# Performance work log

Hardware: AMD Instinct MI355X
Metric: run time of the kernel (lower is better)

The kernel has to match this reference:

```python
import jax, jax.numpy as jnp
import numpy as np

D = 512
H = 8
DH = D // H
DFF = 2048
SLOTS = 1024
TOPK = 5
LN_EPS = 1e-5
NORM_EPS = 1e-12


def setup_inputs() -> dict:
    key = jax.random.key(0)
    ks = jax.random.split(key, 12)
    B, S = 8, 1024
    inp = {
        "src": jax.random.normal(ks[0], (B, S, D), dtype=jnp.float32),
        # MultiheadAttention params (torch layout: in_proj [3D, D], out_proj [D, D])
        "in_proj_w": jax.random.normal(ks[1], (3 * D, D), dtype=jnp.float32) * 0.02,
        "in_proj_b": jnp.zeros((3 * D,), dtype=jnp.float32),
        "out_proj_w": jax.random.normal(ks[2], (D, D), dtype=jnp.float32) * 0.02,
        "out_proj_b": jnp.zeros((D,), dtype=jnp.float32),
        # BPBookMemory params
        "memory": jax.random.normal(ks[3], (SLOTS, D), dtype=jnp.float32),
        "retrieval_scale": jnp.asarray(0.1, dtype=jnp.float32),
        # LayerNorms
        "ln1_g": jnp.ones((D,), dtype=jnp.float32),
        "ln1_b": jnp.zeros((D,), dtype=jnp.float32),
        "ln2_g": jnp.ones((D,), dtype=jnp.float32),
        "ln2_b": jnp.zeros((D,), dtype=jnp.float32),
        # FFN (torch Linear layout: [out, in])
        "w1": jax.random.normal(ks[4], (DFF, D), dtype=jnp.float32) * 0.02,
        "b1": jnp.zeros((DFF,), dtype=jnp.float32),
        "w2": jax.random.normal(ks[5], (D, DFF), dtype=jnp.float32) * 0.02,
        "b2": jnp.zeros((D,), dtype=jnp.float32),
    }
    return inp


def _layer_norm(x, g, b):
    mu = jnp.mean(x, axis=-1, keepdims=True)
    var = jnp.var(x, axis=-1, keepdims=True)
    return (x - mu) * jax.lax.rsqrt(var + LN_EPS) * g + b


def _l2_normalize(x):
    n = jnp.linalg.norm(x, axis=-1, keepdims=True)
    return x / jnp.maximum(n, NORM_EPS)


def _forward(src, in_proj_w, in_proj_b, out_proj_w, out_proj_b,
             memory, retrieval_scale, ln1_g, ln1_b, ln2_g, ln2_b,
             w1, b1, w2, b2):
    B, S, _ = src.shape
    # ---- pre-norm self-attention ----
    h = _layer_norm(src, ln1_g, ln1_b)
    qkv = h @ in_proj_w.T + in_proj_b            # [B,S,3D]
    q, k, v = jnp.split(qkv, 3, axis=-1)
    q = q.reshape(B, S, H, DH)
    k = k.reshape(B, S, H, DH)
    v = v.reshape(B, S, H, DH)
    scores = jnp.einsum("bqhd,bkhd->bhqk", q, k) / jnp.sqrt(jnp.float32(DH))
    attn = jax.nn.softmax(scores, axis=-1)
    ctx = jnp.einsum("bhqk,bkhd->bqhd", attn, v).reshape(B, S, D)
    attn_out = ctx @ out_proj_w.T + out_proj_b
    src = src + attn_out
    # ---- BP-Book memory: cosine sim -> topk -> softmax -> gather -> weighted sum ----
    xn = _l2_normalize(src)                      # [B,S,D]
    mn = _l2_normalize(memory)                   # [SLOTS,D]
    sim = xn @ mn.T                              # [B,S,SLOTS]
    topk_scores, topk_idx = jax.lax.top_k(sim, TOPK)
    w = jax.nn.softmax(topk_scores, axis=-1)     # [B,S,TOPK]
    retrieved = memory[topk_idx]                 # [B,S,TOPK,D]
    weighted = jnp.einsum("bskd,bsk->bsd", retrieved, w)
    src = src + retrieval_scale * weighted
    # ---- FFN ----
    h = _layer_norm(src, ln2_g, ln2_b)
    ffn = jax.nn.gelu(h @ w1.T + b1, approximate=False) @ w2.T + b2
    return src + ffn


def reference(src, in_proj_w, in_proj_b, out_proj_w, out_proj_b,
              memory, retrieval_scale, ln1_g, ln1_b, ln2_g, ln2_b,
              w1, b1, w2, b2):
    return _forward(src, in_proj_w, in_proj_b, out_proj_w, out_proj_b,
                    memory, retrieval_scale, ln1_g, ln1_b, ln2_g, ln2_b,
                    w1, b1, w2, b2)
```

## Files before the change

kernel.cpp:

```cpp
#include <hip/hip_runtime.h>
#include <math.h>

#define D_ 512
#define H_ 8
#define DFF_ 2048
#define SLOTS_ 1024
#define TOPK_ 5
#define NCAND_ 8
#define NTOK_ 8192
#define SEQ_ 1024
#define LN_EPS_ 1e-5f

typedef __attribute__((ext_vector_type(8))) short bf16x8;
typedef __attribute__((ext_vector_type(4))) float f32x4;
typedef __attribute__((ext_vector_type(4))) unsigned u32x4;

__device__ inline void split2(float x, unsigned short& hi, unsigned short& lo) {
    unsigned u = __builtin_bit_cast(unsigned, x);
    hi = (unsigned short)(u >> 16);
    float h = __builtin_bit_cast(float, u & 0xFFFF0000u);
    float rem = x - h;
    lo = (unsigned short)(__builtin_bit_cast(unsigned, rem) >> 16);
}

__device__ __forceinline__ void gld16(const void* g, void* l) {
    __builtin_amdgcn_global_load_lds(
        (const __attribute__((address_space(1))) void*)g,
        (__attribute__((address_space(3))) void*)l, 16, 0, 0);
}

__device__ __forceinline__ int SW7(int r) { return (r ^ (r >> 3)) & 7; }
__device__ __forceinline__ const bf16x8* frag(const unsigned short* p, int r, int c) {
    return (const bf16x8*)(p + r * 64 + ((c ^ SW7(r)) << 3));
}

__global__ __launch_bounds__(256) void split_kernel(
    const float* __restrict__ x, unsigned short* __restrict__ hi,
    unsigned short* __restrict__ lo, int n)
{
    const int i = (blockIdx.x * 256 + threadIdx.x) * 4;
    if (i >= n) return;
    const float4 v = *(const float4*)(x + i);
    const float vv[4] = {v.x, v.y, v.z, v.w};
    unsigned short h[4], l[4];
#pragma unroll
    for (int e = 0; e < 4; ++e) split2(vv[e], h[e], l[e]);
    hi[i + 0] = h[0]; hi[i + 1] = h[1]; hi[i + 2] = h[2]; hi[i + 3] = h[3];
    if (lo) { lo[i + 0] = l[0]; lo[i + 1] = l[1]; lo[i + 2] = l[2]; lo[i + 3] = l[3]; }
}

template <int WLO>
__global__ __launch_bounds__(256) void ln_kernel(
    const float* __restrict__ x, const float* __restrict__ g,
    const float* __restrict__ be, unsigned short* __restrict__ yh,
    unsigned short* __restrict__ yl)
{
    const int row = blockIdx.x;
    const int t = threadIdx.x;
    const float a = x[(size_t)row * D_ + t];
    const float b = x[(size_t)row * D_ + t + 256];
    float s = a + b;
    float ss = a * a + b * b;
#pragma unroll
    for (int off = 32; off; off >>= 1) {
        s += __shfl_xor(s, off);
        ss += __shfl_xor(ss, off);
    }
    __shared__ float rs[4], rss[4];
    if ((t & 63) == 0) { rs[t >> 6] = s; rss[t >> 6] = ss; }
    __syncthreads();
    s = rs[0] + rs[1] + rs[2] + rs[3];
    ss = rss[0] + rss[1] + rss[2] + rss[3];
    const float mu = s * (1.0f / D_);
    const float var = ss * (1.0f / D_) - mu * mu;
    const float r = rsqrtf(var + LN_EPS_);
    const float y0 = (a - mu) * r * g[t] + be[t];
    const float y1 = (b - mu) * r * g[t + 256] + be[t + 256];
    unsigned short h0, l0, h1, l1;
    split2(y0, h0, l0);
    split2(y1, h1, l1);
    yh[(size_t)row * D_ + t] = h0;
    yh[(size_t)row * D_ + t + 256] = h1;
    if (WLO) {
        yl[(size_t)row * D_ + t] = l0;
        yl[(size_t)row * D_ + t + 256] = l1;
    }
}

__global__ __launch_bounds__(64) void mn_kernel(
    const float* __restrict__ mem, float* __restrict__ mn,
    unsigned short* __restrict__ mnh, unsigned short* __restrict__ mnl)
{
    const int row = blockIdx.x;
    const int lane = threadIdx.x;
    float v[8];
    float ss = 0.0f;
#pragma unroll
    for (int j = 0; j < 8; ++j) {
        v[j] = mem[(size_t)row * D_ + j * 64 + lane];
        ss += v[j] * v[j];
    }
#pragma unroll
    for (int off = 32; off; off >>= 1) ss += __shfl_xor(ss, off);
    const float inv = 1.0f / fmaxf(sqrtf(ss), 1e-12f);
#pragma unroll
    for (int j = 0; j < 8; ++j) {
        const float y = v[j] * inv;
        mn[(size_t)row * D_ + j * 64 + lane] = y;
        unsigned short h, l;
        split2(y, h, l);
        mnh[(size_t)row * D_ + j * 64 + lane] = h;
        mnl[(size_t)row * D_ + j * 64 + lane] = l;
    }
}

__global__ __launch_bounds__(64) void rownorm_kernel(
    const float* __restrict__ x, float* __restrict__ invn)
{
    const int row = blockIdx.x;
    const int lane = threadIdx.x;
    float ss = 0.0f;
#pragma unroll
    for (int j = 0; j < 8; ++j) {
        const float v = x[(size_t)row * D_ + j * 64 + lane];
        ss += v * v;
    }
#pragma unroll
    for (int off = 32; off; off >>= 1) ss += __shfl_xor(ss, off);
    if (lane == 0) invn[row] = 1.0f / fmaxf(sqrtf(ss), 1e-12f);
}

enum { EP_QKV = 0, EP_OUTPROJ = 1, EP_SIM = 2, EP_FFN1 = 3, EP_FFN2 = 4 };

template <int SPLIT, int MODE>
__global__ __launch_bounds__(256) void gemm_mf(
    const unsigned short* __restrict__ Ahg, const unsigned short* __restrict__ Alg,
    const unsigned short* __restrict__ Bhg, const unsigned short* __restrict__ Blg,
    const float* __restrict__ bias, const float* __restrict__ res,
    const float* __restrict__ rowscale, float* __restrict__ C,
    unsigned short* __restrict__ Ch, unsigned short* __restrict__ Cl,
    int M, int N, int K)
{
    __shared__ __align__(16) unsigned short sm[(SPLIT == 3 ? 4 : 2) * 8192];
    unsigned short* Ah = sm;
    unsigned short* Al = sm + 8192;
    unsigned short* Bh = sm + (SPLIT == 3 ? 16384 : 8192);
    unsigned short* Bl = sm + 24576;

    const int tid = threadIdx.x;
    const int lane = tid & 63;
    const int w = tid >> 6;
    const int wr = w >> 1, wc = w & 1;
    const int g = lane >> 4, ln = lane & 15;
    const int m0 = blockIdx.x * 128, n0 = blockIdx.y * 128;
    const int lrow8 = lane >> 3, lchunk = lane & 7;

    const unsigned short* gsrc;
    unsigned short* lds;
    int rbase, rofs, nblk;
    if (SPLIT == 3) {
        nblk = 16; rofs = 0;
        if (w == 0)      { gsrc = Ahg; lds = Ah; rbase = m0; }
        else if (w == 1) { gsrc = Alg; lds = Al; rbase = m0; }
        else if (w == 2) { gsrc = Bhg; lds = Bh; rbase = n0; }
        else             { gsrc = Blg; lds = Bl; rbase = n0; }
    } else {
        nblk = 8; rofs = (w & 1) * 64;
        if (w < 2) { gsrc = Ahg; lds = Ah; rbase = m0; }
        else       { gsrc = Bhg; lds = Bh; rbase = n0; }
    }

    f32x4 acc[4][4];
#pragma unroll
    for (int i = 0; i < 4; ++i)
#pragma unroll
        for (int j = 0; j < 4; ++j) acc[i][j] = (f32x4){0.f, 0.f, 0.f, 0.f};

    for (int k0 = 0; k0 < K; k0 += 64) {
#pragma unroll
        for (int blk = 0; blk < nblk; ++blk) {
            const int row = rofs + blk * 8 + lrow8;
            const int sc = lchunk ^ SW7(row);
            gld16(gsrc + (size_t)(rbase + row) * K + k0 + sc * 8,
                  lds + (rofs + blk * 8) * 64);
        }
        __syncthreads();

#pragma unroll
        for (int ks = 0; ks < 2; ++ks) {
            bf16x8 a_h[4], a_l[4], b_h[4], b_l[4];
#pragma unroll
            for (int mi = 0; mi < 4; ++mi) {
                a_h[mi] = *frag(Ah, wr * 64 + mi * 16 + ln, ks * 4 + g);
                if (SPLIT == 3) a_l[mi] = *frag(Al, wr * 64 + mi * 16 + ln, ks * 4 + g);
            }
#pragma unroll
            for (int ni = 0; ni < 4; ++ni) {
                b_h[ni] = *frag(Bh, wc * 64 + ni * 16 + ln, ks * 4 + g);
                if (SPLIT == 3) b_l[ni] = *frag(Bl, wc * 64 + ni * 16 + ln, ks * 4 + g);
            }
#pragma unroll
            for (int mi = 0; mi < 4; ++mi)
#pragma unroll
                for (int ni = 0; ni < 4; ++ni) {
                    acc[mi][ni] = __builtin_amdgcn_mfma_f32_16x16x32_bf16(
                        a_h[mi], b_h[ni], acc[mi][ni], 0, 0, 0);
                    if (SPLIT == 3) {
                        acc[mi][ni] = __builtin_amdgcn_mfma_f32_16x16x32_bf16(
                            a_h[mi], b_l[ni], acc[mi][ni], 0, 0, 0);
                        acc[mi][ni] = __builtin_amdgcn_mfma_f32_16x16x32_bf16(
                            a_l[mi], b_h[ni], acc[mi][ni], 0, 0, 0);
                    }
                }
        }
        __syncthreads();
    }

#pragma unroll
    for (int mi = 0; mi < 4; ++mi) {
#pragma unroll
        for (int ni = 0; ni < 4; ++ni) {
            const int gn = n0 + wc * 64 + ni * 16 + ln;
            const float bz = (MODE == EP_SIM) ? 0.0f : bias[gn];
#pragma unroll
            for (int r2 = 0; r2 < 4; ++r2) {
                const int gm = m0 + wr * 64 + mi * 16 + g * 4 + r2;
                float v = acc[mi][ni][r2];
                if (MODE == EP_SIM) {
                    v *= rowscale[gm];
                    C[(size_t)gm * N + gn] = v;
                } else if (MODE == EP_QKV) {
                    v += bz;
                    if (gn < D_) v *= 0.125f;
                    unsigned short h16, l16;
                    split2(v, h16, l16);
                    Ch[(size_t)gm * N + gn] = h16;
                    Cl[(size_t)gm * N + gn] = l16;
                } else if (MODE == EP_OUTPROJ) {
                    v += bz + res[(size_t)gm * N + gn];
                    C[(size_t)gm * N + gn] = v;
                    unsigned short h16, l16;
                    split2(v, h16, l16);
                    Ch[(size_t)gm * N + gn] = h16;
                    Cl[(size_t)gm * N + gn] = l16;
                } else if (MODE == EP_FFN1) {
                    v += bz;
                    v = 0.5f * v * (1.0f + erff(v * 0.70710678118654752f));
                    unsigned short h16, l16;
                    split2(v, h16, l16);
                    Ch[(size_t)gm * N + gn] = h16;
                } else {
                    v += bz + res[(size_t)gm * N + gn];
                    C[(size_t)gm * N + gn] = v;
                }
            }
        }
    }
}

__global__ __launch_bounds__(256, 2) void attn_kernel(
    const unsigned short* __restrict__ qkvh, const unsigned short* __restrict__ qkvl,
    unsigned short* __restrict__ ctxh, unsigned short* __restrict__ ctxl)
{
    const int id = blockIdx.x;
    const int bh = id & 63;
    const int qt = id >> 6;
    const int b = bh >> 3, h = bh & 7;
    const int tok0 = b * SEQ_ + qt * 128;
    const int kbase0 = b * SEQ_;
    const int tid = threadIdx.x;
    const int lane = tid & 63;
    const int w = tid >> 6;
    const int ln = lane & 15, g = lane >> 4;
    const int lrow8 = lane >> 3, lchunk = lane & 7;

    __shared__ __align__(16) unsigned char smb[65536];
    unsigned*       PP  = (unsigned*)smb;
    unsigned short* Qh  = (unsigned short*)smb;
    unsigned short* Ql  = (unsigned short*)(smb + 16384);
    unsigned short* Kh  = (unsigned short*)(smb + 32768);
    unsigned short* Kl  = (unsigned short*)(smb + 40960);
    unsigned short* Vth = (unsigned short*)(smb + 49152);
    unsigned short* Vtl = (unsigned short*)(smb + 57344);

    const int qoff = h * 64, koff = 512 + h * 64, voff = 1024 + h * 64;

#pragma unroll
    for (int blk = 0; blk < 4; ++blk) {
        const int row = w * 32 + blk * 8 + lrow8;
        const int sc = lchunk ^ SW7(row);
        gld16(qkvh + (size_t)(tok0 + row) * 1536 + qoff + sc * 8,
              Qh + (w * 32 + blk * 8) * 64);
        gld16(qkvl + (size_t)(tok0 + row) * 1536 + qoff + sc * 8,
              Ql + (w * 32 + blk * 8) * 64);
    }
    __syncthreads();
    bf16x8 qfh[2][2], qfl[2][2];
#pragma unroll
    for (int mi = 0; mi < 2; ++mi)
#pragma unroll
        for (int ks = 0; ks < 2; ++ks) {
            qfh[mi][ks] = *frag(Qh, w * 32 + mi * 16 + ln, ks * 4 + g);
            qfl[mi][ks] = *frag(Ql, w * 32 + mi * 16 + ln, ks * 4 + g);
        }

    f32x4 o[2][4];
#pragma unroll
    for (int mi = 0; mi < 2; ++mi)
#pragma unroll
        for (int ni = 0; ni < 4; ++ni) o[mi][ni] = (f32x4){0.f, 0.f, 0.f, 0.f};
    float mrow[2][4], lrow[2][4];
#pragma unroll
    for (int mi = 0; mi < 2; ++mi)
#pragma unroll
        for (int r2 = 0; r2 < 4; ++r2) { mrow[mi][r2] = -INFINITY; lrow[mi][r2] = 0.f; }

    const int p2 = tid & 31, dc = tid >> 5;

    for (int kt = 0; kt < 16; ++kt) {
        const int kb2 = kbase0 + kt * 64;
#pragma unroll
        for (int blk = 0; blk < 2; ++blk) {
            const int row = w * 16 + blk * 8 + lrow8;
            const int sc = lchunk ^ SW7(row);
            gld16(qkvh + (size_t)(kb2 + row) * 1536 + koff + sc * 8,
                  Kh + (w * 16 + blk * 8) * 64);
            gld16(qkvl + (size_t)(kb2 + row) * 1536 + koff + sc * 8,
                  Kl + (w * 16 + blk * 8) * 64);
        }
        {
            const size_t b0 = (size_t)(kb2 + 2 * p2) * 1536 + voff + dc * 8;
            const bf16x8 h0 = *(const bf16x8*)(qkvh + b0);
            const bf16x8 h1 = *(const bf16x8*)(qkvh + b0 + 1536);
            const bf16x8 l0 = *(const bf16x8*)(qkvl + b0);
            const bf16x8 l1 = *(const bf16x8*)(qkvl + b0 + 1536);
#pragma unroll
            for (int j = 0; j < 8; ++j) {
                const int d = dc * 8 + j;
                const int idx = d * 64 + (((p2 >> 2) ^ SW7(d)) << 3) + ((p2 & 3) << 1);
                *(unsigned*)&Vth[idx] = (unsigned)(unsigned short)h0[j]
                                      | ((unsigned)(unsigned short)h1[j] << 16);
                *(unsigned*)&Vtl[idx] = (unsigned)(unsigned short)l0[j]
                                      | ((unsigned)(unsigned short)l1[j] << 16);
            }
        }
        __syncthreads();

        f32x4 s[2][4];
#pragma unroll
        for (int mi = 0; mi < 2; ++mi)
#pragma unroll
            for (int ni = 0; ni < 4; ++ni) s[mi][ni] = (f32x4){0.f, 0.f, 0.f, 0.f};
#pragma unroll
        for (int ks = 0; ks < 2; ++ks) {
            bf16x8 kbh[4], kbl[4];
#pragma unroll
            for (int ni = 0; ni < 4; ++ni) {
                kbh[ni] = *frag(Kh, ni * 16 + ln, ks * 4 + g);
                kbl[ni] = *frag(Kl, ni * 16 + ln, ks * 4 + g);
            }
#pragma unroll
            for (int mi = 0; mi < 2; ++mi)
#pragma unroll
                for (int ni = 0; ni < 4; ++ni) {
                    s[mi][ni] = __builtin_amdgcn_mfma_f32_16x16x32_bf16(qfh[mi][ks], kbh[ni], s[mi][ni], 0, 0, 0);
                    s[mi][ni] = __builtin_amdgcn_mfma_f32_16x16x32_bf16(qfh[mi][ks], kbl[ni], s[mi][ni], 0, 0, 0);
                    s[mi][ni] = __builtin_amdgcn_mfma_f32_16x16x32_bf16(qfl[mi][ks], kbh[ni], s[mi][ni], 0, 0, 0);
                }
        }

        float tm[2][4];
#pragma unroll
        for (int mi = 0; mi < 2; ++mi)
#pragma unroll
            for (int r2 = 0; r2 < 4; ++r2)
                tm[mi][r2] = fmaxf(fmaxf(s[mi][0][r2], s[mi][1][r2]),
                                   fmaxf(s[mi][2][r2], s[mi][3][r2]));
#pragma unroll
        for (int off = 1; off < 16; off <<= 1)
#pragma unroll
            for (int mi = 0; mi < 2; ++mi)
#pragma unroll
                for (int r2 = 0; r2 < 4; ++r2)
                    tm[mi][r2] = fmaxf(tm[mi][r2], __shfl_xor(tm[mi][r2], off));

        float alpha[2][4], psum[2][4];
#pragma unroll
        for (int mi = 0; mi < 2; ++mi)
#pragma unroll
            for (int r2 = 0; r2 < 4; ++r2) {
                const float mnew = fmaxf(mrow[mi][r2], tm[mi][r2]);
                alpha[mi][r2] = __expf(mrow[mi][r2] - mnew);
                mrow[mi][r2] = mnew;
                psum[mi][r2] = 0.f;
            }
#pragma unroll
        for (int mi = 0; mi < 2; ++mi)
#pragma unroll
            for (int ni = 0; ni < 4; ++ni)
#pragma unroll
                for (int r2 = 0; r2 < 4; ++r2) {
                    const float p = __expf(s[mi][ni][r2] - mrow[mi][r2]);
                    psum[mi][r2] += p;
                    unsigned short h16, l16;
                    split2(p, h16, l16);
                    const int prow = w * 32 + mi * 16 + g * 4 + r2;
                    PP[prow * 64 + (((2 * ni + (ln >> 3)) ^ SW7(prow)) << 3) + (ln & 7)]
                        = (unsigned)h16 | ((unsigned)l16 << 16);
                }
#pragma unroll
        for (int off = 1; off < 16; off <<= 1)
#pragma unroll
            for (int mi = 0; mi < 2; ++mi)
#pragma unroll
                for (int r2 = 0; r2 < 4; ++r2)
                    psum[mi][r2] += __shfl_xor(psum[mi][r2], off);
#pragma unroll
        for (int mi = 0; mi < 2; ++mi)
#pragma unroll
            for (int r2 = 0; r2 < 4; ++r2)
                lrow[mi][r2] = lrow[mi][r2] * alpha[mi][r2] + psum[mi][r2];
#pragma unroll
        for (int mi = 0; mi < 2; ++mi)
#pragma unroll
            for (int ni = 0; ni < 4; ++ni)
#pragma unroll
                for (int r2 = 0; r2 < 4; ++r2)
                    o[mi][ni][r2] *= alpha[mi][r2];

#pragma unroll
        for (int ks = 0; ks < 2; ++ks) {
            bf16x8 pah[2], pal[2];
#pragma unroll
            for (int mi = 0; mi < 2; ++mi) {
                const int r = w * 32 + mi * 16 + ln;
                const unsigned* pp = PP + r * 64 + (((ks * 4 + g) ^ SW7(r)) << 3);
                const u32x4 q0 = *(const u32x4*)pp;
                const u32x4 q1 = *(const u32x4*)(pp + 4);
                u32x4 hu, lu;
                hu[0] = __builtin_amdgcn_perm(q0[1], q0[0], 0x05040100u);
                hu[1] = __builtin_amdgcn_perm(q0[3], q0[2], 0x05040100u);
                hu[2] = __builtin_amdgcn_perm(q1[1], q1[0], 0x05040100u);
                hu[3] = __builtin_amdgcn_perm(q1[3], q1[2], 0x05040100u);
                lu[0] = __builtin_amdgcn_perm(q0[1], q0[0], 0x07060302u);
                lu[1] = __builtin_amdgcn_perm(q0[3], q0[2], 0x07060302u);
                lu[2] = __builtin_amdgcn_perm(q1[1], q1[0], 0x07060302u);
                lu[3] = __builtin_amdgcn_perm(q1[3], q1[2], 0x07060302u);
                pah[mi] = __builtin_bit_cast(bf16x8, hu);
                pal[mi] = __builtin_bit_cast(bf16x8, lu);
            }
#pragma unroll
            for (int ni = 0; ni < 4; ++ni) {
                const bf16x8 vbh = *frag(Vth, ni * 16 + ln, ks * 4 + g);
                const bf16x8 vbl = *frag(Vtl, ni * 16 + ln, ks * 4 + g);
#pragma unroll
                for (int mi = 0; mi < 2; ++mi) {
                    o[mi][ni] = __builtin_amdgcn_mfma_f32_16x16x32_bf16(pah[mi], vbh, o[mi][ni], 0, 0, 0);
                    o[mi][ni] = __builtin_amdgcn_mfma_f32_16x16x32_bf16(pah[mi], vbl, o[mi][ni], 0, 0, 0);
                    o[mi][ni] = __builtin_amdgcn_mfma_f32_16x16x32_bf16(pal[mi], vbh, o[mi][ni], 0, 0, 0);
                }
            }
        }
        __syncthreads();
    }

#pragma unroll
    for (int mi = 0; mi < 2; ++mi)
#pragma unroll
        for (int r2 = 0; r2 < 4; ++r2) {
            const float inv = 1.0f / lrow[mi][r2];
            const int row = tok0 + w * 32 + mi * 16 + g * 4 + r2;
#pragma unroll
            for (int ni = 0; ni < 4; ++ni) {
                const float v = o[mi][ni][r2] * inv;
                unsigned short h16, l16;
                split2(v, h16, l16);
                ctxh[(size_t)row * D_ + h * 64 + ni * 16 + ln] = h16;
                ctxl[(size_t)row * D_ + h * 64 + ni * 16 + ln] = l16;
            }
        }
}

__global__ __launch_bounds__(64) void topk_kernel(
    const float* __restrict__ sim, const float* __restrict__ src2,
    const float* __restrict__ mn, const float* __restrict__ mem,
    const float* __restrict__ rs_ptr, float* __restrict__ out)
{
    const int row = blockIdx.x;
    const int lane = threadIdx.x;
    float v[16];
#pragma unroll
    for (int j = 0; j < 16; ++j)
        v[j] = sim[(size_t)row * SLOTS_ + j * 64 + lane];

    int ci[NCAND_];
#pragma unroll
    for (int t = 0; t < NCAND_; ++t) {
        float bv = -INFINITY;
        int bi = 0x7fffffff;
#pragma unroll
        for (int j = 0; j < 16; ++j) {
            const int idx = j * 64 + lane;
            if (v[j] > bv) { bv = v[j]; bi = idx; }
        }
#pragma unroll
        for (int off = 32; off; off >>= 1) {
            const float ov = __shfl_xor(bv, off);
            const int oi = __shfl_xor(bi, off);
            if (ov > bv || (ov == bv && oi < bi)) { bv = ov; bi = oi; }
        }
        ci[t] = bi;
#pragma unroll
        for (int j = 0; j < 16; ++j)
            if (j * 64 + lane == bi) v[j] = -INFINITY;
    }

    float x[8];
    float ss = 0.0f;
#pragma unroll
    for (int j = 0; j < 8; ++j) {
        x[j] = src2[(size_t)row * D_ + j * 64 + lane];
        ss += x[j] * x[j];
    }
#pragma unroll
    for (int off = 32; off; off >>= 1) ss += __shfl_xor(ss, off);
    const float invn = 1.0f / fmaxf(sqrtf(ss), 1e-12f);

    float rv[NCAND_];
#pragma unroll
    for (int t = 0; t < NCAND_; ++t) {
        const float* mrow = mn + (size_t)ci[t] * D_;
        float acc = 0.0f;
#pragma unroll
        for (int j = 0; j < 8; ++j)
            acc = fmaf(x[j], mrow[j * 64 + lane], acc);
#pragma unroll
        for (int off = 32; off; off >>= 1) acc += __shfl_xor(acc, off);
        rv[t] = acc * invn;
    }

    float wv[TOPK_];
    int wi[TOPK_];
    bool used[NCAND_];
#pragma unroll
    for (int t = 0; t < NCAND_; ++t) used[t] = false;
#pragma unroll
    for (int t = 0; t < TOPK_; ++t) {
        float bv = -INFINITY;
        int bi = 0x7fffffff, bu = 0;
#pragma unroll
        for (int u = 0; u < NCAND_; ++u) {
            if (!used[u] && (rv[u] > bv || (rv[u] == bv && ci[u] < bi))) {
                bv = rv[u]; bi = ci[u]; bu = u;
            }
        }
        used[bu] = true;
        wv[t] = bv;
        wi[t] = bi;
    }

    float m = wv[0];
#pragma unroll
    for (int t = 1; t < TOPK_; ++t) m = fmaxf(m, wv[t]);
    float w[TOPK_], ssum = 0.0f;
#pragma unroll
    for (int t = 0; t < TOPK_; ++t) { w[t] = expf(wv[t] - m); ssum += w[t]; }
    const float scale = rs_ptr[0] / ssum;

#pragma unroll
    for (int j = 0; j < 8; ++j) {
        const int d = j * 64 + lane;
        float acc = 0.0f;
#pragma unroll
        for (int t = 0; t < TOPK_; ++t)
            acc += w[t] * mem[(size_t)wi[t] * D_ + d];
        out[(size_t)row * D_ + d] = x[j] + scale * acc;
    }
}

extern "C" void kernel_launch(void* const* d_in, const int* in_sizes, int n_in,
                              void* d_out, int out_size, void* d_ws, size_t ws_size,
                              hipStream_t stream)
{
    const float* src  = (const float*)d_in[0];
    const float* inw  = (const float*)d_in[1];
    const float* inb  = (const float*)d_in[2];
    const float* outw = (const float*)d_in[3];
    const float* outb = (const float*)d_in[4];
    const float* mem  = (const float*)d_in[5];
    const float* rs   = (const float*)d_in[6];
    const float* ln1g = (const float*)d_in[7];
    const float* ln1b = (const float*)d_in[8];
    const float* ln2g = (const float*)d_in[9];
    const float* ln2b = (const float*)d_in[10];
    const float* w1   = (const float*)d_in[11];
    const float* b1   = (const float*)d_in[12];
    const float* w2   = (const float*)d_in[13];
    const float* b2   = (const float*)d_in[14];
    float* out = (float*)d_out;
    char* ws = (char*)d_ws;
    const size_t MB = 1024ull * 1024ull;
    typedef unsigned short u16;

    float* mn   = (float*)(ws + 0);
    u16* mnh    = (u16*)(ws + 2 * MB);
    u16* mnl    = (u16*)(ws + 3 * MB);
    u16* inwh   = (u16*)(ws + 4 * MB);
    u16* inwl   = (u16*)(ws + 5 * MB + 512 * 1024);
    u16* outwh  = (u16*)(ws + 7 * MB);
    u16* outwl  = (u16*)(ws + 7 * MB + 512 * 1024);
    u16* w1h    = (u16*)(ws + 8 * MB);
    u16* w2h    = (u16*)(ws + 10 * MB);
    float* invn = (float*)(ws + 12 * MB);
    u16* hh     = (u16*)(ws + 13 * MB);
    u16* hl     = (u16*)(ws + 21 * MB);
    u16* qkvh   = (u16*)(ws + 29 * MB);
    u16* qkvl   = (u16*)(ws + 53 * MB);
    u16* ctxh   = (u16*)(ws + 13 * MB);
    u16* ctxl   = (u16*)(ws + 21 * MB);
    float* sim  = (float*)(ws + 13 * MB);
    float* src2 = (float*)(ws + 45 * MB);
    u16* src2h  = (u16*)(ws + 61 * MB);
    u16* src2l  = (u16*)(ws + 69 * MB);
    u16* h2h    = (u16*)(ws + 13 * MB);
    u16* Gbf    = (u16*)(ws + 21 * MB);

    split_kernel<<<dim3(768), dim3(256), 0, stream>>>(inw, inwh, inwl, 3 * D_ * D_);
    split_kernel<<<dim3(256), dim3(256), 0, stream>>>(outw, outwh, outwl, D_ * D_);
    split_kernel<<<dim3(1024), dim3(256), 0, stream>>>(w1, w1h, nullptr, DFF_ * D_);
    split_kernel<<<dim3(1024), dim3(256), 0, stream>>>(w2, w2h, nullptr, D_ * DFF_);
    mn_kernel<<<dim3(SLOTS_), dim3(64), 0, stream>>>(mem, mn, mnh, mnl);
    ln_kernel<1><<<dim3(NTOK_), dim3(256), 0, stream>>>(src, ln1g, ln1b, hh, hl);
    gemm_mf<3, EP_QKV><<<dim3(64, 12), dim3(256), 0, stream>>>(
        hh, hl, inwh, inwl, inb, nullptr, nullptr, nullptr, qkvh, qkvl, NTOK_, 1536, 512);
    attn_kernel<<<dim3(512), dim3(256), 0, stream>>>(qkvh, qkvl, ctxh, ctxl);
    gemm_mf<3, EP_OUTPROJ><<<dim3(64, 4), dim3(256), 0, stream>>>(
        ctxh, ctxl, outwh, outwl, outb, src, nullptr, src2, src2h, src2l, NTOK_, 512, 512);
    rownorm_kernel<<<dim3(NTOK_), dim3(64), 0, stream>>>(src2, invn);
    gemm_mf<3, EP_SIM><<<dim3(64, 8), dim3(256), 0, stream>>>(
        src2h, src2l, mnh, mnl, nullptr, nullptr, invn, sim, nullptr, nullptr, NTOK_, 1024, 512);
    topk_kernel<<<dim3(NTOK_), dim3(64), 0, stream>>>(sim, src2, mn, mem, rs, out);
    ln_kernel<0><<<dim3(NTOK_), dim3(256), 0, stream>>>(out, ln2g, ln2b, h2h, nullptr);
    gemm_mf<1, EP_FFN1><<<dim3(64, 16), dim3(256), 0, stream>>>(
        h2h, nullptr, w1h, nullptr, b1, nullptr, nullptr, nullptr, Gbf, nullptr, NTOK_, 2048, 512);
    gemm_mf<1, EP_FFN2><<<dim3(64, 4), dim3(256), 0, stream>>>(
        Gbf, nullptr, w2h, nullptr, b2, out, nullptr, out, nullptr, nullptr, NTOK_, 512, 2048);
}
```

Measured before the change: 337.2 us.

## Fuse LN2 into top-k, drop rownorm, merge weight splits, restructure attention MFMA

Merges the four weight-split launches into one kernel and fuses the second LayerNorm into the top-k/retrieval kernel, which removes a full pass over the activations. The row-norm kernel and the per-row scaling of the similarity matrix are dropped, because top-k ranking within a row does not change under a positive row scale; this relies on top_k recomputing the exact scores for its candidates. The attention kernel is reorganised: the MFMA operands are swapped so that K/V supply the A fragments, row reductions need only two cross-lane shuffles, P is written to LDS as vectors, s_setprio is placed around the MFMA blocks, and ctx is staged through LDS for coalesced 16-byte stores. Workspace buffers are moved to make room for h2h, which now reuses the memory of the QKV weight split.

```diff
diff --git a/kernel.cpp b/kernel.cpp
--- a/kernel.cpp
+++ b/kernel.cpp
@@ -34,22 +34,31 @@
     return (const bf16x8*)(p + r * 64 + ((c ^ SW7(r)) << 3));
 }
 
-__global__ __launch_bounds__(256) void split_kernel(
-    const float* __restrict__ x, unsigned short* __restrict__ hi,
-    unsigned short* __restrict__ lo, int n)
+__global__ __launch_bounds__(256) void splitall_kernel(
+    const float* __restrict__ inw, const float* __restrict__ outw,
+    const float* __restrict__ w1, const float* __restrict__ w2,
+    unsigned short* __restrict__ inwh, unsigned short* __restrict__ inwl,
+    unsigned short* __restrict__ outwh, unsigned short* __restrict__ outwl,
+    unsigned short* __restrict__ w1h, unsigned short* __restrict__ w2h)
 {
     const int i = (blockIdx.x * 256 + threadIdx.x) * 4;
-    if (i >= n) return;
-    const float4 v = *(const float4*)(x + i);
+    const float* x;
+    unsigned short *hh, *ll;
+    int base;
+    if (i < 786432)       { x = inw;  hh = inwh;  ll = inwl;  base = 0; }
+    else if (i < 1048576) { x = outw; hh = outwh; ll = outwl; base = 786432; }
+    else if (i < 2097152) { x = w1;   hh = w1h;   ll = nullptr; base = 1048576; }
+    else                  { x = w2;   hh = w2h;   ll = nullptr; base = 2097152; }
+    const int j = i - base;
+    const float4 v = *(const float4*)(x + j);
     const float vv[4] = {v.x, v.y, v.z, v.w};
     unsigned short h[4], l[4];
 #pragma unroll
     for (int e = 0; e < 4; ++e) split2(vv[e], h[e], l[e]);
-    hi[i + 0] = h[0]; hi[i + 1] = h[1]; hi[i + 2] = h[2]; hi[i + 3] = h[3];
-    if (lo) { lo[i + 0] = l[0]; lo[i + 1] = l[1]; lo[i + 2] = l[2]; lo[i + 3] = l[3]; }
-}
-
-template <int WLO>
+    hh[j + 0] = h[0]; hh[j + 1] = h[1]; hh[j + 2] = h[2]; hh[j + 3] = h[3];
+    if (ll) { ll[j + 0] = l[0]; ll[j + 1] = l[1]; ll[j + 2] = l[2]; ll[j + 3] = l[3]; }
+}
+
 __global__ __launch_bounds__(256) void ln_kernel(
     const float* __restrict__ x, const float* __restrict__ g,
     const float* __restrict__ be, unsigned short* __restrict__ yh,
@@ -81,10 +90,8 @@
     split2(y1, h1, l1);
     yh[(size_t)row * D_ + t] = h0;
     yh[(size_t)row * D_ + t + 256] = h1;
-    if (WLO) {
-        yl[(size_t)row * D_ + t] = l0;
-        yl[(size_t)row * D_ + t + 256] = l1;
-    }
+    yl[(size_t)row * D_ + t] = l0;
+    yl[(size_t)row * D_ + t + 256] = l1;
 }
 
 __global__ __launch_bounds__(64) void mn_kernel(
@@ -114,22 +121,6 @@
     }
 }
 
-__global__ __launch_bounds__(64) void rownorm_kernel(
-    const float* __restrict__ x, float* __restrict__ invn)
-{
-    const int row = blockIdx.x;
-    const int lane = threadIdx.x;
-    float ss = 0.0f;
-#pragma unroll
-    for (int j = 0; j < 8; ++j) {
-        const float v = x[(size_t)row * D_ + j * 64 + lane];
-        ss += v * v;
-    }
-#pragma unroll
-    for (int off = 32; off; off >>= 1) ss += __shfl_xor(ss, off);
-    if (lane == 0) invn[row] = 1.0f / fmaxf(sqrtf(ss), 1e-12f);
-}
-
 enum { EP_QKV = 0, EP_OUTPROJ = 1, EP_SIM = 2, EP_FFN1 = 3, EP_FFN2 = 4 };
 
 template <int SPLIT, int MODE>
@@ -137,7 +128,7 @@
     const unsigned short* __restrict__ Ahg, const unsigned short* __restrict__ Alg,
     const unsigned short* __restrict__ Bhg, const unsigned short* __restrict__ Blg,
     const float* __restrict__ bias, const float* __restrict__ res,
-    const float* __restrict__ rowscale, float* __restrict__ C,
+    float* __restrict__ C,
     unsigned short* __restrict__ Ch, unsigned short* __restrict__ Cl,
     int M, int N, int K)
 {
@@ -227,7 +218,6 @@
                 const int gm = m0 + wr * 64 + mi * 16 + g * 4 + r2;
                 float v = acc[mi][ni][r2];
                 if (MODE == EP_SIM) {
-                    v *= rowscale[gm];
                     C[(size_t)gm * N + gn] = v;
                 } else if (MODE == EP_QKV) {
                     v += bz;
@@ -297,23 +287,21 @@
     __syncthreads();
     bf16x8 qfh[2][2], qfl[2][2];
 #pragma unroll
-    for (int mi = 0; mi < 2; ++mi)
+    for (int qi = 0; qi < 2; ++qi)
 #pragma unroll
         for (int ks = 0; ks < 2; ++ks) {
-            qfh[mi][ks] = *frag(Qh, w * 32 + mi * 16 + ln, ks * 4 + g);
-            qfl[mi][ks] = *frag(Ql, w * 32 + mi * 16 + ln, ks * 4 + g);
-        }
-
-    f32x4 o[2][4];
-#pragma unroll
-    for (int mi = 0; mi < 2; ++mi)
-#pragma unroll
-        for (int ni = 0; ni < 4; ++ni) o[mi][ni] = (f32x4){0.f, 0.f, 0.f, 0.f};
-    float mrow[2][4], lrow[2][4];
-#pragma unroll
-    for (int mi = 0; mi < 2; ++mi)
-#pragma unroll
-        for (int r2 = 0; r2 < 4; ++r2) { mrow[mi][r2] = -INFINITY; lrow[mi][r2] = 0.f; }
+            qfh[qi][ks] = *frag(Qh, w * 32 + qi * 16 + ln, ks * 4 + g);
+            qfl[qi][ks] = *frag(Ql, w * 32 + qi * 16 + ln, ks * 4 + g);
+        }
+    __syncthreads();
+
+    f32x4 o[4][2];
+#pragma unroll
+    for (int di = 0; di < 4; ++di)
+#pragma unroll
+        for (int qi = 0; qi < 2; ++qi) o[di][qi] = (f32x4){0.f, 0.f, 0.f, 0.f};
+    float mrow2[2] = {-INFINITY, -INFINITY};
+    float lrow2[2] = {0.f, 0.f};
 
     const int p2 = tid & 31, dc = tid >> 5;
 
@@ -346,95 +334,87 @@
         }
         __syncthreads();
 
-        f32x4 s[2][4];
-#pragma unroll
-        for (int mi = 0; mi < 2; ++mi)
-#pragma unroll
-            for (int ni = 0; ni < 4; ++ni) s[mi][ni] = (f32x4){0.f, 0.f, 0.f, 0.f};
+        f32x4 s[4][2];
+#pragma unroll
+        for (int ki = 0; ki < 4; ++ki)
+#pragma unroll
+            for (int qi = 0; qi < 2; ++qi) s[ki][qi] = (f32x4){0.f, 0.f, 0.f, 0.f};
+        __builtin_amdgcn_s_setprio(1);
 #pragma unroll
         for (int ks = 0; ks < 2; ++ks) {
             bf16x8 kbh[4], kbl[4];
 #pragma unroll
-            for (int ni = 0; ni < 4; ++ni) {
-                kbh[ni] = *frag(Kh, ni * 16 + ln, ks * 4 + g);
-                kbl[ni] = *frag(Kl, ni * 16 + ln, ks * 4 + g);
-            }
-#pragma unroll
-            for (int mi = 0; mi < 2; ++mi)
-#pragma unroll
-                for (int ni = 0; ni < 4; ++ni) {
-                    s[mi][ni] = __builtin_amdgcn_mfma_f32_16x16x32_bf16(qfh[mi][ks], kbh[ni], s[mi][ni], 0, 0, 0);
-                    s[mi][ni] = __builtin_amdgcn_mfma_f32_16x16x32_bf16(qfh[mi][ks], kbl[ni], s[mi][ni], 0, 0, 0);
-                    s[mi][ni] = __builtin_amdgcn_mfma_f32_16x16x32_bf16(qfl[mi][ks], kbh[ni], s[mi][ni], 0, 0, 0);
+            for (int ki = 0; ki < 4; ++ki) {
+                kbh[ki] = *frag(Kh, ki * 16 + ln, ks * 4 + g);
+                kbl[ki] = *frag(Kl, ki * 16 + ln, ks * 4 + g);
+            }
+#pragma unroll
+            for (int ki = 0; ki < 4; ++ki)
+#pragma unroll
+                for (int qi = 0; qi < 2; ++qi) {
+                    s[ki][qi] = __builtin_amdgcn_mfma_f32_16x16x32_bf16(kbh[ki], qfh[qi][ks], s[ki][qi], 0, 0, 0);
+                    s[ki][qi] = __builtin_amdgcn_mfma_f32_16x16x32_bf16(kbh[ki], qfl[qi][ks], s[ki][qi], 0, 0, 0);
+                    s[ki][qi] = __builtin_amdgcn_mfma_f32_16x16x32_bf16(kbl[ki], qfh[qi][ks], s[ki][qi], 0, 0, 0);
                 }
         }
-
-        float tm[2][4];
-#pragma unroll
-        for (int mi = 0; mi < 2; ++mi)
-#pragma unroll
-            for (int r2 = 0; r2 < 4; ++r2)
-                tm[mi][r2] = fmaxf(fmaxf(s[mi][0][r2], s[mi][1][r2]),
-                                   fmaxf(s[mi][2][r2], s[mi][3][r2]));
-#pragma unroll
-        for (int off = 1; off < 16; off <<= 1)
-#pragma unroll
-            for (int mi = 0; mi < 2; ++mi)
-#pragma unroll
-                for (int r2 = 0; r2 < 4; ++r2)
-                    tm[mi][r2] = fmaxf(tm[mi][r2], __shfl_xor(tm[mi][r2], off));
-
-        float alpha[2][4], psum[2][4];
-#pragma unroll
-        for (int mi = 0; mi < 2; ++mi)
-#pragma unroll
-            for (int r2 = 0; r2 < 4; ++r2) {
-                const float mnew = fmaxf(mrow[mi][r2], tm[mi][r2]);
-                alpha[mi][r2] = __expf(mrow[mi][r2] - mnew);
-                mrow[mi][r2] = mnew;
-                psum[mi][r2] = 0.f;
-            }
-#pragma unroll
-        for (int mi = 0; mi < 2; ++mi)
-#pragma unroll
-            for (int ni = 0; ni < 4; ++ni)
+        __builtin_amdgcn_s_setprio(0);
+
+        float tm2[2], alpha2[2], psum2[2];
+#pragma unroll
+        for (int qi = 0; qi < 2; ++qi) {
+            float m01 = fmaxf(fmaxf(s[0][qi][0], s[0][qi][1]), fmaxf(s[0][qi][2], s[0][qi][3]));
+            float m23 = fmaxf(fmaxf(s[1][qi][0], s[1][qi][1]), fmaxf(s[1][qi][2], s[1][qi][3]));
+            float m45 = fmaxf(fmaxf(s[2][qi][0], s[2][qi][1]), fmaxf(s[2][qi][2], s[2][qi][3]));
+            float m67 = fmaxf(fmaxf(s[3][qi][0], s[3][qi][1]), fmaxf(s[3][qi][2], s[3][qi][3]));
+            tm2[qi] = fmaxf(fmaxf(m01, m23), fmaxf(m45, m67));
+        }
+#pragma unroll
+        for (int qi = 0; qi < 2; ++qi) {
+            tm2[qi] = fmaxf(tm2[qi], __shfl_xor(tm2[qi], 16));
+            tm2[qi] = fmaxf(tm2[qi], __shfl_xor(tm2[qi], 32));
+            const float mnew = fmaxf(mrow2[qi], tm2[qi]);
+            alpha2[qi] = __expf(mrow2[qi] - mnew);
+            mrow2[qi] = mnew;
+            psum2[qi] = 0.f;
+        }
+#pragma unroll
+        for (int qi = 0; qi < 2; ++qi)
+#pragma unroll
+            for (int ki = 0; ki < 4; ++ki) {
+                u32x4 pv;
 #pragma unroll
                 for (int r2 = 0; r2 < 4; ++r2) {
-                    const float p = __expf(s[mi][ni][r2] - mrow[mi][r2]);
-                    psum[mi][r2] += p;
+                    const float p = __expf(s[ki][qi][r2] - mrow2[qi]);
+                    psum2[qi] += p;
                     unsigned short h16, l16;
                     split2(p, h16, l16);
-                    const int prow = w * 32 + mi * 16 + g * 4 + r2;
-                    PP[prow * 64 + (((2 * ni + (ln >> 3)) ^ SW7(prow)) << 3) + (ln & 7)]
-                        = (unsigned)h16 | ((unsigned)l16 << 16);
+                    pv[r2] = (unsigned)h16 | ((unsigned)l16 << 16);
                 }
-#pragma unroll
-        for (int off = 1; off < 16; off <<= 1)
-#pragma unroll
-            for (int mi = 0; mi < 2; ++mi)
+                *(u32x4*)&PP[(w * 32 + qi * 16 + ln) * 64 + ((ki ^ (ln & 3)) << 4) + (g << 2)] = pv;
+            }
+#pragma unroll
+        for (int qi = 0; qi < 2; ++qi) {
+            psum2[qi] += __shfl_xor(psum2[qi], 16);
+            psum2[qi] += __shfl_xor(psum2[qi], 32);
+            lrow2[qi] = lrow2[qi] * alpha2[qi] + psum2[qi];
+        }
+#pragma unroll
+        for (int di = 0; di < 4; ++di)
+#pragma unroll
+            for (int qi = 0; qi < 2; ++qi)
 #pragma unroll
                 for (int r2 = 0; r2 < 4; ++r2)
-                    psum[mi][r2] += __shfl_xor(psum[mi][r2], off);
-#pragma unroll
-        for (int mi = 0; mi < 2; ++mi)
-#pragma unroll
-            for (int r2 = 0; r2 < 4; ++r2)
-                lrow[mi][r2] = lrow[mi][r2] * alpha[mi][r2] + psum[mi][r2];
-#pragma unroll
-        for (int mi = 0; mi < 2; ++mi)
-#pragma unroll
-            for (int ni = 0; ni < 4; ++ni)
-#pragma unroll
-                for (int r2 = 0; r2 < 4; ++r2)
-                    o[mi][ni][r2] *= alpha[mi][r2];
-
+                    o[di][qi][r2] *= alpha2[qi];
+
+        __builtin_amdgcn_s_setprio(1);
 #pragma unroll
         for (int ks = 0; ks < 2; ++ks) {
             bf16x8 pah[2], pal[2];
 #pragma unroll
-            for (int mi = 0; mi < 2; ++mi) {
-                const int r = w * 32 + mi * 16 + ln;
-                const unsigned* pp = PP + r * 64 + (((ks * 4 + g) ^ SW7(r)) << 3);
+            for (int qi = 0; qi < 2; ++qi) {
+                const int kiR = 2 * ks + (g >> 1);
+                const unsigned* pp = PP + (w * 32 + qi * 16 + ln) * 64
+                                     + (((kiR ^ (ln & 3)) << 4) + ((g & 1) << 3));
                 const u32x4 q0 = *(const u32x4*)pp;
                 const u32x4 q1 = *(const u32x4*)(pp + 4);
                 u32x4 hu, lu;
@@ -446,45 +426,77 @@
                 lu[1] = __builtin_amdgcn_perm(q0[3], q0[2], 0x07060302u);
                 lu[2] = __builtin_amdgcn_perm(q1[1], q1[0], 0x07060302u);
                 lu[3] = __builtin_amdgcn_perm(q1[3], q1[2], 0x07060302u);
-                pah[mi] = __builtin_bit_cast(bf16x8, hu);
-                pal[mi] = __builtin_bit_cast(bf16x8, lu);
-            }
-#pragma unroll
-            for (int ni = 0; ni < 4; ++ni) {
-                const bf16x8 vbh = *frag(Vth, ni * 16 + ln, ks * 4 + g);
-                const bf16x8 vbl = *frag(Vtl, ni * 16 + ln, ks * 4 + g);
-#pragma unroll
-                for (int mi = 0; mi < 2; ++mi) {
-                    o[mi][ni] = __builtin_amdgcn_mfma_f32_16x16x32_bf16(pah[mi], vbh, o[mi][ni], 0, 0, 0);
-                    o[mi][ni] = __builtin_amdgcn_mfma_f32_16x16x32_bf16(pah[mi], vbl, o[mi][ni], 0, 0, 0);
-                    o[mi][ni] = __builtin_amdgcn_mfma_f32_16x16x32_bf16(pal[mi], vbh, o[mi][ni], 0, 0, 0);
+                pah[qi] = __builtin_bit_cast(bf16x8, hu);
+                pal[qi] = __builtin_bit_cast(bf16x8, lu);
+            }
+            bf16x8 vbh[4], vbl[4];
+#pragma unroll
+            for (int di = 0; di < 4; ++di) {
+                vbh[di] = *frag(Vth, di * 16 + ln, ks * 4 + g);
+                vbl[di] = *frag(Vtl, di * 16 + ln, ks * 4 + g);
+            }
+#pragma unroll
+            for (int di = 0; di < 4; ++di)
+#pragma unroll
+                for (int qi = 0; qi < 2; ++qi) {
+                    o[di][qi] = __builtin_amdgcn_mfma_f32_16x16x32_bf16(vbh[di], pah[qi], o[di][qi], 0, 0, 0);
+                    o[di][qi] = __builtin_amdgcn_mfma_f32_16x16x32_bf16(vbh[di], pal[qi], o[di][qi], 0, 0, 0);
+                    o[di][qi] = __builtin_amdgcn_mfma_f32_16x16x32_bf16(vbl[di], pah[qi], o[di][qi], 0, 0, 0);
                 }
-            }
-        }
+        }
+        __builtin_amdgcn_s_setprio(0);
         __syncthreads();
     }
 
 #pragma unroll
-    for (int mi = 0; mi < 2; ++mi)
-#pragma unroll
-        for (int r2 = 0; r2 < 4; ++r2) {
-            const float inv = 1.0f / lrow[mi][r2];
-            const int row = tok0 + w * 32 + mi * 16 + g * 4 + r2;
-#pragma unroll
-            for (int ni = 0; ni < 4; ++ni) {
-                const float v = o[mi][ni][r2] * inv;
+    for (int di = 0; di < 4; ++di)
+#pragma unroll
+        for (int qi = 0; qi < 2; ++qi) {
+            const float inv = 1.0f / lrow2[qi];
+            u32x4 tv;
+#pragma unroll
+            for (int r2 = 0; r2 < 4; ++r2) {
+                const float v = o[di][qi][r2] * inv;
                 unsigned short h16, l16;
                 split2(v, h16, l16);
-                ctxh[(size_t)row * D_ + h * 64 + ni * 16 + ln] = h16;
-                ctxl[(size_t)row * D_ + h * 64 + ni * 16 + ln] = l16;
-            }
-        }
+                tv[r2] = (unsigned)h16 | ((unsigned)l16 << 16);
+            }
+            *(u32x4*)&PP[(w * 32 + qi * 16 + ln) * 64 + ((di ^ (ln & 3)) << 4) + (g << 2)] = tv;
+        }
+    __syncthreads();
+    {
+        const int qrow = lane >> 1, halfd = lane & 1;
+        const size_t gbase = (size_t)(tok0 + w * 32 + qrow) * D_ + h * 64;
+#pragma unroll
+        for (int gi = 0; gi < 2; ++gi) {
+            const int di = halfd * 2 + gi;
+            const unsigned* tp = PP + (w * 32 + qrow) * 64 + ((di ^ (qrow & 3)) << 4);
+#pragma unroll
+            for (int pr = 0; pr < 2; ++pr) {
+                const u32x4 t0 = *(const u32x4*)(tp + pr * 8);
+                const u32x4 t1 = *(const u32x4*)(tp + pr * 8 + 4);
+                u32x4 hv, lv;
+                hv[0] = __builtin_amdgcn_perm(t0[1], t0[0], 0x05040100u);
+                hv[1] = __builtin_amdgcn_perm(t0[3], t0[2], 0x05040100u);
+                hv[2] = __builtin_amdgcn_perm(t1[1], t1[0], 0x05040100u);
+                hv[3] = __builtin_amdgcn_perm(t1[3], t1[2], 0x05040100u);
+                lv[0] = __builtin_amdgcn_perm(t0[1], t0[0], 0x07060302u);
+                lv[1] = __builtin_amdgcn_perm(t0[3], t0[2], 0x07060302u);
+                lv[2] = __builtin_amdgcn_perm(t1[1], t1[0], 0x07060302u);
+                lv[3] = __builtin_amdgcn_perm(t1[3], t1[2], 0x07060302u);
+                *(u32x4*)(ctxh + gbase + di * 16 + pr * 8) = hv;
+                *(u32x4*)(ctxl + gbase + di * 16 + pr * 8) = lv;
+            }
+        }
+    }
 }
 
 __global__ __launch_bounds__(64) void topk_kernel(
     const float* __restrict__ sim, const float* __restrict__ src2,
     const float* __restrict__ mn, const float* __restrict__ mem,
-    const float* __restrict__ rs_ptr, float* __restrict__ out)
+    const float* __restrict__ rs_ptr, const float* __restrict__ g2,
+    const float* __restrict__ b2, float* __restrict__ out,
+    unsigned short* __restrict__ h2h)
 {
     const int row = blockIdx.x;
     const int lane = threadIdx.x;
@@ -567,6 +579,8 @@
     for (int t = 0; t < TOPK_; ++t) { w[t] = expf(wv[t] - m); ssum += w[t]; }
     const float scale = rs_ptr[0] / ssum;
 
+    float y[8];
+    float s_ = 0.f, ss2 = 0.f;
 #pragma unroll
     for (int j = 0; j < 8; ++j) {
         const int d = j * 64 + lane;
@@ -574,7 +588,26 @@
 #pragma unroll
         for (int t = 0; t < TOPK_; ++t)
             acc += w[t] * mem[(size_t)wi[t] * D_ + d];
-        out[(size_t)row * D_ + d] = x[j] + scale * acc;
+        y[j] = x[j] + scale * acc;
+        out[(size_t)row * D_ + d] = y[j];
+        s_ += y[j];
+        ss2 += y[j] * y[j];
+    }
+#pragma unroll
+    for (int off = 32; off; off >>= 1) {
+        s_ += __shfl_xor(s_, off);
+        ss2 += __shfl_xor(ss2, off);
+    }
+    const float mu = s_ * (1.0f / D_);
+    const float var = ss2 * (1.0f / D_) - mu * mu;
+    const float r = rsqrtf(var + LN_EPS_);
+#pragma unroll
+    for (int j = 0; j < 8; ++j) {
+        const int d = j * 64 + lane;
+        const float h2 = (y[j] - mu) * r * g2[d] + b2[d];
+        unsigned short h16, l16;
+        split2(h2, h16, l16);
+        h2h[(size_t)row * D_ + d] = h16;
     }
 }
 
@@ -605,13 +638,13 @@
     float* mn   = (float*)(ws + 0);
     u16* mnh    = (u16*)(ws + 2 * MB);
     u16* mnl    = (u16*)(ws + 3 * MB);
+    u16* h2h    = (u16*)(ws + 4 * MB);
     u16* inwh   = (u16*)(ws + 4 * MB);
     u16* inwl   = (u16*)(ws + 5 * MB + 512 * 1024);
     u16* outwh  = (u16*)(ws + 7 * MB);
     u16* outwl  = (u16*)(ws + 7 * MB + 512 * 1024);
-    u16* w1h    = (u16*)(ws + 8 * MB);
-    u16* w2h    = (u16*)(ws + 10 * MB);
-    float* invn = (float*)(ws + 12 * MB);
+    u16* w1h    = (u16*)(ws + 77 * MB);
+    u16* w2h    = (u16*)(ws + 79 * MB);
     u16* hh     = (u16*)(ws + 13 * MB);
     u16* hl     = (u16*)(ws + 21 * MB);
     u16* qkvh   = (u16*)(ws + 29 * MB);
@@ -622,27 +655,23 @@
     float* src2 = (float*)(ws + 45 * MB);
     u16* src2h  = (u16*)(ws + 61 * MB);
     u16* src2l  = (u16*)(ws + 69 * MB);
-    u16* h2h    = (u16*)(ws + 13 * MB);
     u16* Gbf    = (u16*)(ws + 21 * MB);
 
-    split_kernel<<<dim3(768), dim3(256), 0, stream>>>(inw, inwh, inwl, 3 * D_ * D_);
-    split_kernel<<<dim3(256), dim3(256), 0, stream>>>(outw, outwh, outwl, D_ * D_);
-    split_kernel<<<dim3(1024), dim3(256), 0, stream>>>(w1, w1h, nullptr, DFF_ * D_);
-    split_kernel<<<dim3(1024), dim3(256), 0, stream>>>(w2, w2h, nullptr, D_ * DFF_);
+    splitall_kernel<<<dim3(3072), dim3(256), 0, stream>>>(
+        inw, outw, w1, w2, inwh, inwl, outwh, outwl, w1h, w2h);
     mn_kernel<<<dim3(SLOTS_), dim3(64), 0, stream>>>(mem, mn, mnh, mnl);
-    ln_kernel<1><<<dim3(NTOK_), dim3(256), 0, stream>>>(src, ln1g, ln1b, hh, hl);
+    ln_kernel<<<dim3(NTOK_), dim3(256), 0, stream>>>(src, ln1g, ln1b, hh, hl);
     gemm_mf<3, EP_QKV><<<dim3(64, 12), dim3(256), 0, stream>>>(
-        hh, hl, inwh, inwl, inb, nullptr, nullptr, nullptr, qkvh, qkvl, NTOK_, 1536, 512);
+        hh, hl, inwh, inwl, inb, nullptr, nullptr, qkvh, qkvl, NTOK_, 1536, 512);
     attn_kernel<<<dim3(512), dim3(256), 0, stream>>>(qkvh, qkvl, ctxh, ctxl);
     gemm_mf<3, EP_OUTPROJ><<<dim3(64, 4), dim3(256), 0, stream>>>(
-        ctxh, ctxl, outwh, outwl, outb, src, nullptr, src2, src2h, src2l, NTOK_, 512, 512);
-    rownorm_kernel<<<dim3(NTOK_), dim3(64), 0, stream>>>(src2, invn);
+        ctxh, ctxl, outwh, outwl, outb, src, src2, src2h, src2l, NTOK_, 512, 512);
     gemm_mf<3, EP_SIM><<<dim3(64, 8), dim3(256), 0, stream>>>(
-        src2h, src2l, mnh, mnl, nullptr, nullptr, invn, sim, nullptr, nullptr, NTOK_, 1024, 512);
-    topk_kernel<<<dim3(NTOK_), dim3(64), 0, stream>>>(sim, src2, mn, mem, rs, out);
-    ln_kernel<0><<<dim3(NTOK_), dim3(256), 0, stream>>>(out, ln2g, ln2b, h2h, nullptr);
+        src2h, src2l, mnh, mnl, nullptr, nullptr, sim, nullptr, nullptr, NTOK_, 1024, 512);
+    topk_kernel<<<dim3(NTOK_), dim3(64), 0, stream>>>(
+        sim, src2, mn, mem, rs, ln2g, ln2b, out, h2h);
     gemm_mf<1, EP_FFN1><<<dim3(64, 16), dim3(256), 0, stream>>>(
-        h2h, nullptr, w1h, nullptr, b1, nullptr, nullptr, nullptr, Gbf, nullptr, NTOK_, 2048, 512);
+        h2h, nullptr, w1h, nullptr, b1, nullptr, nullptr, Gbf, nullptr, NTOK_, 2048, 512);
     gemm_mf<1, EP_FFN2><<<dim3(64, 4), dim3(256), 0, stream>>>(
-        Gbf, nullptr, w2h, nullptr, b2, out, nullptr, out, nullptr, nullptr, NTOK_, 512, 2048);
-}
+        Gbf, nullptr, w2h, nullptr, b2, out, out, nullptr, nullptr, NTOK_, 512, 2048);
+}
```

New measurement: 302.9 us. 10.2% less time.
